# Optimization experiments

Hardware: AMD Instinct MI355X
Metric: run time of the kernel (lower is better)

Reference implementation:

```python
import jax, jax.numpy as jnp
import numpy as np

T, K, F = 131072, 64, 8
EPS = 1e-10


def setup_inputs() -> dict:
    key = jax.random.key(0)
    k0, k1, k2, k3 = jax.random.split(key, 4)
    return {
        "observations": jax.random.normal(k0, (T, F), dtype=jnp.float32),
        "beta_logits": jax.random.normal(k1, (K,), dtype=jnp.float32),
        "pi_logits": jax.random.normal(k2, (K, K), dtype=jnp.float32),
        "means": 0.1 * jax.random.normal(k3, (K, F), dtype=jnp.float32),
        "log_vars": jnp.zeros((K, F), dtype=jnp.float32),
    }


def _stick_breaking(logits):
    betas = jax.nn.sigmoid(logits)
    cp = jnp.cumprod(1.0 - betas)
    return betas * jnp.concatenate([jnp.ones((1,), betas.dtype), cp[:-1]])


def _emission_log_probs(obs, means, log_vars):
    # Diagonal-covariance MVN log-prob, vectorized over (T, K) via matmuls
    # logN(x; mu, diag(v)) = -0.5 * (sum((x-mu)^2/v) + sum(log v) + F*log(2pi))
    inv_var = jnp.exp(-log_vars)                                 # (K, F)
    quad = (obs ** 2) @ inv_var.T                                # (T, K): sum x^2/v
    cross = obs @ (means * inv_var).T                            # (T, K): sum x*mu/v
    const = jnp.sum(means ** 2 * inv_var + log_vars, axis=1)     # (K,)
    log2pi = jnp.float32(np.log(2.0 * np.pi))
    Fdim = obs.shape[1]
    return -0.5 * (quad - 2.0 * cross + const[None, :] + Fdim * log2pi)


def reference(observations, beta_logits, pi_logits, means, log_vars):
    beta_w = _stick_breaking(beta_logits)                        # (K,)
    trans = jax.nn.softmax(pi_logits, axis=1)                    # (K, K)
    em = jnp.exp(_emission_log_probs(observations, means, log_vars))  # (T, K)

    # Forward recursion
    a0 = beta_w * em[0]
    a0 = a0 / (a0.sum() + EPS)

    def fwd_step(a, e):
        a = (a @ trans) * e
        a = a / (a.sum() + EPS)
        return a, a

    _, alpha_rest = jax.lax.scan(fwd_step, a0, em[1:])
    alpha = jnp.concatenate([a0[None, :], alpha_rest], axis=0)   # (T, K)

    # Backward recursion: beta[t] = normalize(trans @ (beta[t+1] * em[t+1]))
    bT = jnp.ones((trans.shape[0],), observations.dtype)

    def bwd_step(b, e_next):
        b = trans @ (b * e_next)
        b = b / (b.sum() + EPS)
        return b, b

    _, beta_rev = jax.lax.scan(bwd_step, bT, em[1:], reverse=True)
    beta = jnp.concatenate([beta_rev, bT[None, :]], axis=0)      # (T, K)

    log_likelihood = jnp.log(alpha[-1].sum() + EPS)
    return alpha, beta, log_likelihood
```

## Files before the change

### kernel.cpp

```cpp
#include <hip/hip_runtime.h>

#define T_N   131072
#define K_N   64
#define L_C   128
#define F_N   8
#define N_CH  (T_N / L_C)
#define WARM  96
#define EPS_F 1e-10f
#define OBS_MAX ((T_N - 1) * F_N)

#define LOG2E 1.4426950408889634f
#define NL2E  (-0.72134752044448170f)
#define LN2   0.6931471805599453f
#define LN2PI 1.8378770664093453f
#define EMSC  16.0f

typedef float v2f __attribute__((ext_vector_type(2)));
typedef unsigned uint2v __attribute__((ext_vector_type(2)));

#define DPPI(SRC, CTRL) __builtin_amdgcn_update_dpp(0, (SRC), (CTRL), 0xF, 0xF, true)
#define DPPF(SRC, CTRL) __int_as_float(DPPI(__float_as_int(SRC), (CTRL)))

template <int CTRL>
__device__ __forceinline__ float dpp_add(float x) {
  int y = __builtin_amdgcn_update_dpp(0, __float_as_int(x), CTRL, 0xF, 0xF, true);
  return x + __int_as_float(y);
}
__device__ __forceinline__ float wave_sum64(float x) {
  x = dpp_add<0x111>(x);
  x = dpp_add<0x112>(x);
  x = dpp_add<0x114>(x);
  x = dpp_add<0x118>(x);
  x = dpp_add<0x142>(x);
  x = dpp_add<0x143>(x);
  return __int_as_float(__builtin_amdgcn_readlane(__float_as_int(x), 63));
}

#if __has_builtin(__builtin_amdgcn_permlane16_swap) && \
    __has_builtin(__builtin_amdgcn_permlane32_swap)
__device__ __forceinline__ float psum16(float x) {
  uint2v r = __builtin_amdgcn_permlane16_swap(__float_as_uint(x),
                                              __float_as_uint(x), false, false);
  return __uint_as_float(r.x) + __uint_as_float(r.y);
}
__device__ __forceinline__ float psum32(float x) {
  uint2v r = __builtin_amdgcn_permlane32_swap(__float_as_uint(x),
                                              __float_as_uint(x), false, false);
  return __uint_as_float(r.x) + __uint_as_float(r.y);
}
#else
__device__ __forceinline__ float psum16(float x) {
  return x + __int_as_float(
      __builtin_amdgcn_ds_swizzle(__float_as_int(x), 0x401F));
}
__device__ __forceinline__ float psum32(float x) {
  int addr = (((int)threadIdx.x ^ 32) & 63) << 2;
  return x + __int_as_float(
      __builtin_amdgcn_ds_bpermute(addr, __float_as_int(x)));
}
#endif

#define PKFMA(a, b, c) __builtin_elementwise_fma(a, b, c)

__device__ __forceinline__ float em_pk(const float4& xa, const float4& xb,
                                       const v2f civ2[4], const v2f cmiv2[4],
                                       float cc) {
  v2f x0 = {xa.x, xa.y}, x1 = {xa.z, xa.w};
  v2f x2 = {xb.x, xb.y}, x3 = {xb.z, xb.w};
  v2f a0 = {cc, 0.f}, a1 = {0.f, 0.f};
  a0 = PKFMA(x0, PKFMA(x0, civ2[0], cmiv2[0]), a0);
  a1 = PKFMA(x1, PKFMA(x1, civ2[1], cmiv2[1]), a1);
  a0 = PKFMA(x2, PKFMA(x2, civ2[2], cmiv2[2]), a0);
  a1 = PKFMA(x3, PKFMA(x3, civ2[3], cmiv2[3]), a1);
  v2f s = a0 + a1;
  return __builtin_amdgcn_exp2f(s.x + s.y);
}

#define MATVEC(VV, MOUT)                                                      \
  {                                                                           \
    float Gr[16];                                                             \
    Gr[0] = (VV);                                                             \
    Gr[1] = DPPF(Gr[0], 0xB1);                                 \
    Gr[2] = DPPF(Gr[0], 0x4E);                                 \
    Gr[3] = DPPF(Gr[1], 0x4E);                                                \
    _Pragma("unroll")                                                         \
    for (int rr = 0; rr < 4; ++rr) Gr[4 + rr] = DPPF(Gr[rr], 0x124);          \
    _Pragma("unroll")                                                         \
    for (int rr = 0; rr < 8; ++rr) Gr[8 + rr] = DPPF(Gr[rr], 0x128);          \
    v2f aE0 = {0.f,0.f}, aE1 = {0.f,0.f}, aO0 = {0.f,0.f}, aO1 = {0.f,0.f};   \
    _Pragma("unroll")                                                         \
    for (int rr = 0; rr < 8; ++rr) {                                          \
      v2f gg = {Gr[rr], Gr[rr]};                                              \
      aE0 = PKFMA(gg, TcE[rr], aE0);                                          \
      aO0 = PKFMA(gg, TcO[rr], aO0);                                          \
    }                                                                         \
    _Pragma("unroll")                                                         \
    for (int rr = 8; rr < 16; ++rr) {                                         \
      v2f gg = {Gr[rr], Gr[rr]};                                              \
      aE1 = PKFMA(gg, TcE[rr], aE1);                                          \
      aO1 = PKFMA(gg, TcO[rr], aO1);                                          \
    }                                                                         \
    v2f accE = aE0 + aE1, accO = aO0 + aO1;           \
    float pe0 = psum32(accE.x), pe2 = psum32(accE.y);                         \
    float po1 = psum32(accO.x), po3 = psum32(accO.y);                         \
    pe0 = psum16(pe0); pe2 = psum16(pe2);                                     \
    po1 = psum16(po1); po3 = psum16(po3);                                     \
    float tE = qb1 ? pe2 : pe0;                                               \
    float tO = qb1 ? po3 : po1;                                               \
    MOUT = qb0 ? tO : tE;                                                     \
  }

extern "C" __global__ void __launch_bounds__(64, 2)
hdphmm_fb(const float* __restrict__ obs,
          const float* __restrict__ beta_logits,
          const float* __restrict__ pi_logits,
          const float* __restrict__ means,
          const float* __restrict__ log_vars,
          float* __restrict__ out) {
  const int lane = threadIdx.x;
  const int bid  = blockIdx.x;
  const int h    = lane & 15;
  const bool qb0 = (lane >> 4) & 1;
  const bool qb1 = (lane >> 5) & 1;
  __shared__ __align__(8) float2 sstat[K_N];
  __shared__ float sb[K_N];

  float* alpha   = out;
  float* betaout = out + (size_t)T_N * K_N;

  v2f civ2[4], cmiv2[4];
  float c0, cw;
  {
    const float4* mp = reinterpret_cast<const float4*>(means + lane * F_N);
    const float4* lp = reinterpret_cast<const float4*>(log_vars + lane * F_N);
    float4 m0 = mp[0], m1 = mp[1];
    float4 l0 = lp[0], l1 = lp[1];
    float mu[8] = {m0.x, m0.y, m0.z, m0.w, m1.x, m1.y, m1.z, m1.w};
    float lv[8] = {l0.x, l0.y, l0.z, l0.w, l1.x, l1.y, l1.z, l1.w};
    float cst = F_N * LN2PI;
#pragma unroll
    for (int f = 0; f < 8; ++f) {
      float iv = __builtin_amdgcn_exp2f(-lv[f] * LOG2E);
      cst += lv[f] + mu[f] * mu[f] * iv;
      float cf  = NL2E * iv;
      civ2[f >> 1][f & 1]  = cf;
      cmiv2[f >> 1][f & 1] = -2.0f * mu[f] * cf;
    }
    c0 = NL2E * cst;
    cw = c0 + EMSC;
  }

  {
    const float4* pr4 = reinterpret_cast<const float4*>(pi_logits + lane * K_N);
    float mx = -3.0e38f;
#pragma unroll
    for (int k = 0; k < 16; ++k) {
      float4 r = pr4[k];
      mx = fmaxf(mx, fmaxf(fmaxf(r.x, r.y), fmaxf(r.z, r.w)));
    }
    float s = 0.0f;
#pragma unroll
    for (int k = 0; k < 16; ++k) {
      float4 r = pr4[k];
      s += __builtin_amdgcn_exp2f((r.x - mx) * LOG2E);
      s += __builtin_amdgcn_exp2f((r.y - mx) * LOG2E);
      s += __builtin_amdgcn_exp2f((r.z - mx) * LOG2E);
      s += __builtin_amdgcn_exp2f((r.w - mx) * LOG2E);
    }
    sstat[lane] = make_float2(mx, __builtin_amdgcn_rcpf(s));
  }
  __syncthreads();

  int ki[16];
  ki[0] = lane;
  ki[1] = DPPI(ki[0], 0xB1);
  ki[2] = DPPI(ki[0], 0x4E);
  ki[3] = DPPI(ki[1], 0x4E);
#pragma unroll
  for (int rr = 0; rr < 4; ++rr) ki[4 + rr] = DPPI(ki[rr], 0x124);
#pragma unroll
  for (int rr = 0; rr < 8; ++rr) ki[8 + rr] = DPPI(ki[rr], 0x128);

  if (bid < N_CH) {
    v2f TcE[16], TcO[16];
#pragma unroll
    for (int rr = 0; rr < 16; ++rr) {
      int k = ki[rr];
      float2 st = sstat[k];
      const float* pk = pi_logits + k * K_N;
      float e0 = __builtin_amdgcn_exp2f((pk[h]      - st.x) * LOG2E) * st.y;
      float e1 = __builtin_amdgcn_exp2f((pk[h + 16] - st.x) * LOG2E) * st.y;
      float e2 = __builtin_amdgcn_exp2f((pk[h + 32] - st.x) * LOG2E) * st.y;
      float e3 = __builtin_amdgcn_exp2f((pk[h + 48] - st.x) * LOG2E) * st.y;
      TcE[rr] = (v2f){e0, e2};
      TcO[rr] = (v2f){e1, e3};
    }

    const int out_lo = bid * L_C;
    float v;
    int t_first;
    if (bid == 0) {
      float bl = beta_logits[lane];
      float ex = __builtin_amdgcn_exp2f(-bl * LOG2E);
      float bw = __builtin_amdgcn_rcpf(1.0f + ex);
      sb[lane] = 1.0f - bw;
      __syncthreads();
      float pr = 1.0f;
#pragma unroll
      for (int i = 0; i < 64; ++i) {
        float qv = sb[i];
        pr = (i < lane) ? pr * qv : pr;
      }
      float4 x0 = reinterpret_cast<const float4*>(obs)[0];
      float4 x1 = reinterpret_cast<const float4*>(obs)[1];
      v = bw * pr * em_pk(x0, x1, civ2, cmiv2, c0);
      t_first = 1;
    } else {
      const int t0 = out_lo - WARM;
      const float4* xp = reinterpret_cast<const float4*>(obs + t0 * F_N);
      v = em_pk(xp[0], xp[1], civ2, cmiv2, cw);
      t_first = t0 + 1;
    }
    int obs_off = t_first * F_N;
    float4 xa, xb;
    {
      const float4* xp = reinterpret_cast<const float4*>(obs + obs_off);
      xa = xp[0]; xb = xp[1];
    }
    int out_off = out_lo * K_N + lane;

    const int wn8 = (bid == 0) ? 0 : (WARM >> 3);
#pragma unroll 1
    for (int o = 0; o < wn8; ++o) {
#pragma unroll
      for (int i = 0; i < 8; ++i) {
        float4 nxa = *reinterpret_cast<const float4*>(obs + obs_off + F_N);
        float4 nxb = *reinterpret_cast<const float4*>(obs + obs_off + F_N + 4);
        float m;
        MATVEC(v, m)
        float e = em_pk(xa, xb, civ2, cmiv2, cw);
        v = m * e;
        xa = nxa; xb = nxb; obs_off += F_N;
      }
      float Sw = wave_sum64(v);
      v *= __builtin_amdgcn_rcpf(Sw);
    }

    float S = wave_sum64(v);
    float r_st = __builtin_amdgcn_rcpf(S + EPS_F);

#define FWD_SSTEP                                                             \
  {                                                                           \
    int offn = obs_off + F_N; offn = (offn > OBS_MAX) ? OBS_MAX : offn;       \
    float4 nxa = *reinterpret_cast<const float4*>(obs + offn);                \
    float4 nxb = *reinterpret_cast<const float4*>(obs + offn + 4);            \
    float m;                                                                  \
    MATVEC(v, m)                                                              \
    alpha[out_off] = v * r_st; out_off += K_N;                                \
    float e = em_pk(xa, xb, civ2, cmiv2, c0);                                 \
    float vn = m * (r_st * e);                                                \
    S = wave_sum64(vn);                                                       \
    r_st = __builtin_amdgcn_rcpf(S + EPS_F);                                  \
    v = vn; xa = nxa; xb = nxb; obs_off = offn;                               \
  }

#pragma unroll 2
    for (int it = 0; it < L_C - 1; ++it) FWD_SSTEP
#undef FWD_SSTEP
    alpha[out_off] = v * r_st;
    if (bid == N_CH - 1 && lane == 0) {
      float sl = S * r_st + EPS_F;
      out[(size_t)2 * T_N * K_N] = __builtin_amdgcn_logf(sl) * LN2;
    }
  } else {
    v2f TcE[16], TcO[16];
    {
      float2 s0 = sstat[h], s1 = sstat[h + 16];
      float2 s2 = sstat[h + 32], s3 = sstat[h + 48];
#pragma unroll
      for (int rr = 0; rr < 16; ++rr) {
        int k = ki[rr];
        float p0 = pi_logits[h * K_N + k];
        float p1 = pi_logits[(h + 16) * K_N + k];
        float p2 = pi_logits[(h + 32) * K_N + k];
        float p3 = pi_logits[(h + 48) * K_N + k];
        TcE[rr] = (v2f){__builtin_amdgcn_exp2f((p0 - s0.x) * LOG2E) * s0.y,
                        __builtin_amdgcn_exp2f((p2 - s2.x) * LOG2E) * s2.y};
        TcO[rr] = (v2f){__builtin_amdgcn_exp2f((p1 - s1.x) * LOG2E) * s1.y,
                        __builtin_amdgcn_exp2f((p3 - s3.x) * LOG2E) * s3.y};
      }
    }
    const int cb   = bid - N_CH;
    const int t_lo = cb * L_C;
    const int t_hi = t_lo + L_C - 1;
    int t_top = t_hi + WARM;
    if (t_top > T_N - 1) t_top = T_N - 1;
    const int s_top = (cb == N_CH - 1) ? T_N - 2 : t_hi;

    float w;
    {
      const float4* xp = reinterpret_cast<const float4*>(obs + t_top * F_N);
      w = em_pk(xp[0], xp[1], civ2, cmiv2, cw);
    }
    if (cb == N_CH - 1)
      betaout[(size_t)(T_N - 1) * K_N + lane] = 1.0f;
    int obs_off = (t_top - 1) * F_N;
    float4 xa, xb;
    {
      const float4* xp = reinterpret_cast<const float4*>(obs + obs_off);
      xa = xp[0]; xb = xp[1];
    }
    int out_off = s_top * K_N + lane;

#define BWD_WSTEP                                                             \
  {                                                                           \
    float4 nxa = *reinterpret_cast<const float4*>(obs + obs_off - F_N);       \
    float4 nxb = *reinterpret_cast<const float4*>(obs + obs_off - F_N + 4);   \
    float m;                                                                  \
    MATVEC(w, m)                                                              \
    float e = em_pk(xa, xb, civ2, cmiv2, cw);                                 \
    w = m * e;                                                                \
    xa = nxa; xb = nxb; obs_off -= F_N;                                       \
  }

    const int pw  = (t_top - s_top) - 1;
    const int pw8 = pw >> 3, pwr = pw & 7;
#pragma unroll 1
    for (int o = 0; o < pw8; ++o) {
#pragma unroll
      for (int i = 0; i < 8; ++i) BWD_WSTEP
      float Sw = wave_sum64(w);
      w *= __builtin_amdgcn_rcpf(Sw);
    }
#pragma unroll 1
    for (int it = 0; it < pwr; ++it) BWD_WSTEP
#undef BWD_WSTEP

    float u, S, r_st;
    {
      float m;
      MATVEC(w, m)
      float Sm = wave_sum64(m);
      u = m * __builtin_amdgcn_rcpf(Sm);
      float e = em_pk(xa, xb, civ2, cmiv2, c0);
      w = u * e;
      S = wave_sum64(u);
      r_st = __builtin_amdgcn_rcpf(S + EPS_F);
      int offn = obs_off - F_N; offn = (offn < 0) ? 0 : offn;
      xa = *reinterpret_cast<const float4*>(obs + offn);
      xb = *reinterpret_cast<const float4*>(obs + offn + 4);
      obs_off = offn;
    }

#define BWD_SSTEP                                                             \
  {                                                                           \
    int offn = obs_off - F_N; offn = (offn < 0) ? 0 : offn;                   \
    float4 nxa = *reinterpret_cast<const float4*>(obs + offn);                \
    float4 nxb = *reinterpret_cast<const float4*>(obs + offn + 4);            \
    float m;                                                                  \
    MATVEC(w, m)                                                              \
    betaout[out_off] = u * r_st; out_off -= K_N;                              \
    float u2 = m * r_st;                                                      \
    float e = em_pk(xa, xb, civ2, cmiv2, c0);                                 \
    w = u2 * e;                                                               \
    S = wave_sum64(u2);                                                       \
    r_st = __builtin_amdgcn_rcpf(S + EPS_F);                                  \
    u = u2; xa = nxa; xb = nxb; obs_off = offn;                               \
  }

    const int store_n = s_top - t_lo;
#pragma unroll 2
    for (int it = 0; it < store_n; ++it) BWD_SSTEP
#undef BWD_SSTEP
    betaout[t_lo * K_N + lane] = u * r_st;
  }
}

extern "C" void kernel_launch(void* const* d_in, const int* in_sizes, int n_in,
                              void* d_out, int out_size, void* d_ws, size_t ws_size,
                              hipStream_t stream) {
  (void)in_sizes; (void)n_in; (void)out_size; (void)d_ws; (void)ws_size;
  const float* obs  = (const float*)d_in[0];
  const float* bl   = (const float*)d_in[1];
  const float* pi   = (const float*)d_in[2];
  const float* mns  = (const float*)d_in[3];
  const float* lvs  = (const float*)d_in[4];
  hipLaunchKernelGGL(hdphmm_fb, dim3(2 * N_CH), dim3(64), 0, stream,
                     obs, bl, pi, mns, lvs, (float*)d_out);
}
```

Before: 181.0 us.

## Replace DPP-based 64x64 matvec with split-bf16 MFMA matvec via LDS

The per-step transition matvec, previously done with DPP broadcasts, packed FMAs and permlane reductions, is recomputed on matrix cores. The vector is split into bf16 hi/lo parts and staged through shared memory. The transition matrix is stored as bf16 hi/lo A fragments, and three MFMA products per tile approximate fp32 accuracy. The result is selected from the accumulator and redistributed with ds_bpermute. This trades VALU and cross-lane work for MFMA latency, an LDS round-trip on the serial recurrence path, and some precision loss from the split-bf16 scheme.

```diff
diff --git a/kernel.cpp b/kernel.cpp
--- a/kernel.cpp
+++ b/kernel.cpp
@@ -16,10 +16,8 @@
 #define EMSC  16.0f
 
 typedef float v2f __attribute__((ext_vector_type(2)));
-typedef unsigned uint2v __attribute__((ext_vector_type(2)));
-
-#define DPPI(SRC, CTRL) __builtin_amdgcn_update_dpp(0, (SRC), (CTRL), 0xF, 0xF, true)
-#define DPPF(SRC, CTRL) __int_as_float(DPPI(__float_as_int(SRC), (CTRL)))
+typedef __attribute__((ext_vector_type(8))) short short8;
+typedef __attribute__((ext_vector_type(4))) float f32x4;
 
 template <int CTRL>
 __device__ __forceinline__ float dpp_add(float x) {
@@ -36,31 +34,16 @@
   return __int_as_float(__builtin_amdgcn_readlane(__float_as_int(x), 63));
 }
 
-#if __has_builtin(__builtin_amdgcn_permlane16_swap) && \
-    __has_builtin(__builtin_amdgcn_permlane32_swap)
-__device__ __forceinline__ float psum16(float x) {
-  uint2v r = __builtin_amdgcn_permlane16_swap(__float_as_uint(x),
-                                              __float_as_uint(x), false, false);
-  return __uint_as_float(r.x) + __uint_as_float(r.y);
-}
-__device__ __forceinline__ float psum32(float x) {
-  uint2v r = __builtin_amdgcn_permlane32_swap(__float_as_uint(x),
-                                              __float_as_uint(x), false, false);
-  return __uint_as_float(r.x) + __uint_as_float(r.y);
-}
-#else
-__device__ __forceinline__ float psum16(float x) {
-  return x + __int_as_float(
-      __builtin_amdgcn_ds_swizzle(__float_as_int(x), 0x401F));
-}
-__device__ __forceinline__ float psum32(float x) {
-  int addr = (((int)threadIdx.x ^ 32) & 63) << 2;
-  return x + __int_as_float(
-      __builtin_amdgcn_ds_bpermute(addr, __float_as_int(x)));
-}
-#endif
-
 #define PKFMA(a, b, c) __builtin_elementwise_fma(a, b, c)
+
+__device__ __forceinline__ unsigned short bf16rn(float x) {
+  unsigned u = __float_as_uint(x);
+  unsigned r = u + 0x7FFFu + ((u >> 16) & 1u);
+  return (unsigned short)(r >> 16);
+}
+__device__ __forceinline__ float ubf(unsigned short b) {
+  return __uint_as_float(((unsigned)b) << 16);
+}
 
 __device__ __forceinline__ float em_pk(const float4& xa, const float4& xb,
                                        const v2f civ2[4], const v2f cmiv2[4],
@@ -76,38 +59,41 @@
   return __builtin_amdgcn_exp2f(s.x + s.y);
 }
 
+#define MFMA16(A, B, C) __builtin_amdgcn_mfma_f32_16x16x32_bf16((A), (B), (C), 0, 0, 0)
+
 #define MATVEC(VV, MOUT)                                                      \
   {                                                                           \
-    float Gr[16];                                                             \
-    Gr[0] = (VV);                                                             \
-    Gr[1] = DPPF(Gr[0], 0xB1);                                 \
-    Gr[2] = DPPF(Gr[0], 0x4E);                                 \
-    Gr[3] = DPPF(Gr[1], 0x4E);                                                \
+    int pkh_, pkl_;                                                           \
+    asm("v_cvt_pk_bf16_f32 %0, %1, %2" : "=v"(pkh_) : "v"(VV), "v"(0.f));     \
+    float hif_ = __uint_as_float(((unsigned)pkh_) << 16);                     \
+    float lof_ = (VV) - hif_;                                                 \
+    asm("v_cvt_pk_bf16_f32 %0, %1, %2" : "=v"(pkl_) : "v"(lof_), "v"(0.f));   \
+    vtab[lane]      = (unsigned short)pkh_;                                   \
+    vtab[64 + lane] = (unsigned short)pkl_;                                   \
+    const short8 Bh0_ = *(const short8*)(vtab      + 8 * g);                  \
+    const short8 Bh1_ = *(const short8*)(vtab + 32 + 8 * g);                  \
+    const short8 Bl0_ = *(const short8*)(vtab + 64 + 8 * g);                  \
+    const short8 Bl1_ = *(const short8*)(vtab + 96 + 8 * g);                  \
+    const f32x4 z4_ = {0.f, 0.f, 0.f, 0.f};                                   \
+    f32x4 accv_[4];                                                           \
     _Pragma("unroll")                                                         \
-    for (int rr = 0; rr < 4; ++rr) Gr[4 + rr] = DPPF(Gr[rr], 0x124);          \
-    _Pragma("unroll")                                                         \
-    for (int rr = 0; rr < 8; ++rr) Gr[8 + rr] = DPPF(Gr[rr], 0x128);          \
-    v2f aE0 = {0.f,0.f}, aE1 = {0.f,0.f}, aO0 = {0.f,0.f}, aO1 = {0.f,0.f};   \
-    _Pragma("unroll")                                                         \
-    for (int rr = 0; rr < 8; ++rr) {                                          \
-      v2f gg = {Gr[rr], Gr[rr]};                                              \
-      aE0 = PKFMA(gg, TcE[rr], aE0);                                          \
-      aO0 = PKFMA(gg, TcO[rr], aO0);                                          \
+    for (int mt_ = 0; mt_ < 4; ++mt_) {                                       \
+      f32x4 aA_ = MFMA16(Ahi[mt_][0], Bh0_, z4_);                             \
+      f32x4 aB_ = MFMA16(Ahi[mt_][1], Bh1_, z4_);                             \
+      aA_ = MFMA16(Alo[mt_][0], Bh0_, aA_);                                   \
+      aB_ = MFMA16(Alo[mt_][1], Bh1_, aB_);                                   \
+      aA_ = MFMA16(Ahi[mt_][0], Bl0_, aA_);                                   \
+      aB_ = MFMA16(Ahi[mt_][1], Bl1_, aB_);                                   \
+      accv_[mt_] = aA_ + aB_;                                                 \
     }                                                                         \
-    _Pragma("unroll")                                                         \
-    for (int rr = 8; rr < 16; ++rr) {                                         \
-      v2f gg = {Gr[rr], Gr[rr]};                                              \
-      aE1 = PKFMA(gg, TcE[rr], aE1);                                          \
-      aO1 = PKFMA(gg, TcO[rr], aO1);                                          \
-    }                                                                         \
-    v2f accE = aE0 + aE1, accO = aO0 + aO1;           \
-    float pe0 = psum32(accE.x), pe2 = psum32(accE.y);                         \
-    float po1 = psum32(accO.x), po3 = psum32(accO.y);                         \
-    pe0 = psum16(pe0); pe2 = psum16(pe2);                                     \
-    po1 = psum16(po1); po3 = psum16(po3);                                     \
-    float tE = qb1 ? pe2 : pe0;                                               \
-    float tO = qb1 ? po3 : po1;                                               \
-    MOUT = qb0 ? tO : tE;                                                     \
+    f32x4 sA_ = mtb0 ? accv_[1] : accv_[0];                                   \
+    f32x4 sB_ = mtb0 ? accv_[3] : accv_[2];                                   \
+    f32x4 sC_ = mtb1 ? sB_ : sA_;                                             \
+    float w01_ = rb0 ? sC_.y : sC_.x;                                         \
+    float w23_ = rb0 ? sC_.w : sC_.z;                                         \
+    float ws_  = rb1 ? w23_ : w01_;                                           \
+    MOUT = __int_as_float(                                                    \
+        __builtin_amdgcn_ds_bpermute(bpx, __float_as_int(ws_)));              \
   }
 
 extern "C" __global__ void __launch_bounds__(64, 2)
@@ -119,11 +105,17 @@
           float* __restrict__ out) {
   const int lane = threadIdx.x;
   const int bid  = blockIdx.x;
-  const int h    = lane & 15;
-  const bool qb0 = (lane >> 4) & 1;
-  const bool qb1 = (lane >> 5) & 1;
+  const int g    = lane >> 4;
+  const int h16  = lane & 15;
+  const bool mtb0 = (lane >> 2) & 1;
+  const bool mtb1 = (lane >> 3) & 1;
+  const bool rb0  = lane & 1;
+  const bool rb1  = (lane >> 1) & 1;
+  const int bpx = (((((lane & 15) >> 2) << 4) | ((lane >> 4) << 2) | (lane & 3)) << 2);
+
   __shared__ __align__(8) float2 sstat[K_N];
   __shared__ float sb[K_N];
+  __shared__ __align__(16) unsigned short vtab[128];
 
   float* alpha   = out;
   float* betaout = out + (size_t)T_N * K_N;
@@ -171,30 +163,27 @@
   }
   __syncthreads();
 
-  int ki[16];
-  ki[0] = lane;
-  ki[1] = DPPI(ki[0], 0xB1);
-  ki[2] = DPPI(ki[0], 0x4E);
-  ki[3] = DPPI(ki[1], 0x4E);
-#pragma unroll
-  for (int rr = 0; rr < 4; ++rr) ki[4 + rr] = DPPI(ki[rr], 0x124);
-#pragma unroll
-  for (int rr = 0; rr < 8; ++rr) ki[8 + rr] = DPPI(ki[rr], 0x128);
+  short8 Ahi[4][2], Alo[4][2];
 
   if (bid < N_CH) {
-    v2f TcE[16], TcO[16];
-#pragma unroll
-    for (int rr = 0; rr < 16; ++rr) {
-      int k = ki[rr];
-      float2 st = sstat[k];
-      const float* pk = pi_logits + k * K_N;
-      float e0 = __builtin_amdgcn_exp2f((pk[h]      - st.x) * LOG2E) * st.y;
-      float e1 = __builtin_amdgcn_exp2f((pk[h + 16] - st.x) * LOG2E) * st.y;
-      float e2 = __builtin_amdgcn_exp2f((pk[h + 32] - st.x) * LOG2E) * st.y;
-      float e3 = __builtin_amdgcn_exp2f((pk[h + 48] - st.x) * LOG2E) * st.y;
-      TcE[rr] = (v2f){e0, e2};
-      TcO[rr] = (v2f){e1, e3};
-    }
+#pragma unroll
+    for (int mt = 0; mt < 4; ++mt)
+#pragma unroll
+      for (int kk = 0; kk < 2; ++kk) {
+        int row = mt * 16 + h16;
+        int kb  = kk * 32 + g * 8;
+#pragma unroll
+        for (int j = 0; j < 8; ++j) {
+          int k = kb + j;
+          float2 st = sstat[k];
+          float tv = __builtin_amdgcn_exp2f(
+                         (pi_logits[(size_t)k * K_N + row] - st.x) * LOG2E) * st.y;
+          unsigned short hb = bf16rn(tv);
+          unsigned short lb = bf16rn(tv - ubf(hb));
+          Ahi[mt][kk][j] = (short)hb;
+          Alo[mt][kk][j] = (short)lb;
+        }
+      }
 
     const int out_lo = bid * L_C;
     float v;
@@ -273,23 +262,26 @@
       out[(size_t)2 * T_N * K_N] = __builtin_amdgcn_logf(sl) * LN2;
     }
   } else {
-    v2f TcE[16], TcO[16];
-    {
-      float2 s0 = sstat[h], s1 = sstat[h + 16];
-      float2 s2 = sstat[h + 32], s3 = sstat[h + 48];
-#pragma unroll
-      for (int rr = 0; rr < 16; ++rr) {
-        int k = ki[rr];
-        float p0 = pi_logits[h * K_N + k];
-        float p1 = pi_logits[(h + 16) * K_N + k];
-        float p2 = pi_logits[(h + 32) * K_N + k];
-        float p3 = pi_logits[(h + 48) * K_N + k];
-        TcE[rr] = (v2f){__builtin_amdgcn_exp2f((p0 - s0.x) * LOG2E) * s0.y,
-                        __builtin_amdgcn_exp2f((p2 - s2.x) * LOG2E) * s2.y};
-        TcO[rr] = (v2f){__builtin_amdgcn_exp2f((p1 - s1.x) * LOG2E) * s1.y,
-                        __builtin_amdgcn_exp2f((p3 - s3.x) * LOG2E) * s3.y};
+#pragma unroll
+    for (int mt = 0; mt < 4; ++mt) {
+      int row = mt * 16 + h16;
+      float2 st = sstat[row];
+#pragma unroll
+      for (int kk = 0; kk < 2; ++kk) {
+        int kb = kk * 32 + g * 8;
+#pragma unroll
+        for (int j = 0; j < 8; ++j) {
+          int k = kb + j;
+          float tv = __builtin_amdgcn_exp2f(
+                         (pi_logits[(size_t)row * K_N + k] - st.x) * LOG2E) * st.y;
+          unsigned short hb = bf16rn(tv);
+          unsigned short lb = bf16rn(tv - ubf(hb));
+          Ahi[mt][kk][j] = (short)hb;
+          Alo[mt][kk][j] = (short)lb;
+        }
       }
     }
+
     const int cb   = bid - N_CH;
     const int t_lo = cb * L_C;
     const int t_hi = t_lo + L_C - 1;
```

Result: slower. 226.3 us (+25.0%).
